# Kernel tuning notes

Measured on AMD Instinct MI355X. Metric: run time of the kernel, lower is better.

## Reference

```python
import jax, jax.numpy as jnp
import numpy as np

N, C, H, W = 16, 64, 128, 128
KH, KW = 3, 3
SH, SW = 1, 1


def _window_flat_indices(H, W):
    """Flat input indices of each element of each sliding window.
    Returns int32 array [num_windows, KH*KW]."""
    Ho = (H - KH) // SH + 1
    Wo = (W - KW) // SW + 1
    i = np.arange(Ho) * SH
    j = np.arange(Wo) * SW
    a = np.arange(KH)
    b = np.arange(KW)
    rows = i[:, None, None, None] + a[None, None, :, None]   # [Ho,1,KH,1]
    cols = j[None, :, None, None] + b[None, None, None, :]   # [1,Wo,1,KW]
    flat = (rows * W + cols).reshape(Ho * Wo, KH * KW)       # [Wn, K]
    return jnp.asarray(flat, dtype=jnp.int32)


def setup_inputs() -> dict:
    key = jax.random.key(0)
    x = jax.random.normal(key, (N, C, H, W), dtype=jnp.float32)
    return {"x": x}


def reference(x):
    n, c, h, w = x.shape
    flat = _window_flat_indices(h, w)            # [Wn, K]
    Wn, K = flat.shape
    nc = n * c
    xf = x.reshape(nc, h * w)                    # [NC, HW]
    patches = xf[:, flat]                        # [NC, Wn, K]
    amax = jnp.argmax(patches, axis=-1)          # [NC, Wn] local winner
    amin = jnp.argmin(patches, axis=-1)          # [NC, Wn]
    warp = jnp.arange(Wn)[None, :]
    win_max = flat[warp, amax]                   # [NC, Wn] flat input idx of max winner
    win_min = flat[warp, amin]                   # [NC, Wn]
    idx = jnp.concatenate([win_max, win_min], axis=1)                      # [NC, 2Wn]
    vals = jnp.concatenate([jnp.ones((Wn,), x.dtype), -jnp.ones((Wn,), x.dtype)])
    counts = jnp.zeros((nc, h * w), x.dtype)
    counts = counts.at[jnp.arange(nc)[:, None], idx].add(vals[None, :])
    return counts.reshape(n, c, h, w)
```

## Files before the change

kernel.cpp:

```cpp
#include <hip/hip_runtime.h>


#define HH 128
#define WW 128
#define HO 126
#define WO 126
#define PLANE (HH * WW)
#define NPLANES (16 * 64)
#define BLOCK 1024
#define CTILES 32
#define RTILES 63
#define NTILES (CTILES * RTILES)

__device__ __forceinline__ void scan9(float w0, float w1, float w2,
                                      float w3, float w4, float w5,
                                      float w6, float w7, float w8,
                                      int base, int* __restrict__ cnt) {
    float vmax = w0, vmin = w0;
    int omax = 0, omin = 0;
#define STEP(v, off)                                      \
    do {                                                  \
        if ((v) > vmax) { vmax = (v); omax = (off); }     \
        if ((v) < vmin) { vmin = (v); omin = (off); }     \
    } while (0)
    STEP(w1, 1);
    STEP(w2, 2);
    STEP(w3, WW);
    STEP(w4, WW + 1);
    STEP(w5, WW + 2);
    STEP(w6, 2 * WW);
    STEP(w7, 2 * WW + 1);
    STEP(w8, 2 * WW + 2);
#undef STEP
    atomicAdd(&cnt[base + omax], 1);
    atomicAdd(&cnt[base + omin], -1);
}

__global__ __launch_bounds__(BLOCK, 8)
void energy_pool2d_kernel(const float* __restrict__ x, float* __restrict__ out) {
    __shared__ int cnt[PLANE];

    const int tid = threadIdx.x;
    const int plane = blockIdx.x;
    const float* __restrict__ xp = x + (size_t)plane * PLANE;

    int4* c4 = (int4*)cnt;
#pragma unroll
    for (int i = 0; i < PLANE / 4 / BLOCK; ++i)
        c4[tid + i * BLOCK] = make_int4(0, 0, 0, 0);
    __syncthreads();

    for (int t = tid; t < NTILES; t += BLOCK) {
        const int rt = t >> 5;
        const int ct = t & 31;
        const int wr0 = rt * 2;
        const int j0 = ct * 4;
        const float* __restrict__ p = xp + wr0 * WW + j0;

        const float4 a0 = *(const float4*)(p);
        const float4 a1 = *(const float4*)(p + WW);
        const float4 a2 = *(const float4*)(p + 2 * WW);
        const float4 a3 = *(const float4*)(p + 3 * WW);
        float4 b0, b1, b2, b3;
        if (ct < CTILES - 1) {
            b0 = *(const float4*)(p + 4);
            b1 = *(const float4*)(p + WW + 4);
            b2 = *(const float4*)(p + 2 * WW + 4);
            b3 = *(const float4*)(p + 3 * WW + 4);
        } else {
            b0 = b1 = b2 = b3 = make_float4(0.f, 0.f, 0.f, 0.f);
        }
        const float r0[8] = {a0.x, a0.y, a0.z, a0.w, b0.x, b0.y, b0.z, b0.w};
        const float r1[8] = {a1.x, a1.y, a1.z, a1.w, b1.x, b1.y, b1.z, b1.w};
        const float r2[8] = {a2.x, a2.y, a2.z, a2.w, b2.x, b2.y, b2.z, b2.w};
        const float r3[8] = {a3.x, a3.y, a3.z, a3.w, b3.x, b3.y, b3.z, b3.w};

        const int nw = (ct < CTILES - 1) ? 4 : 2;
        const int base0 = wr0 * WW + j0;
#pragma unroll
        for (int c = 0; c < 4; ++c) {
            if (c < nw) {
                scan9(r0[c], r0[c + 1], r0[c + 2],
                      r1[c], r1[c + 1], r1[c + 2],
                      r2[c], r2[c + 1], r2[c + 2], base0 + c, cnt);
                scan9(r1[c], r1[c + 1], r1[c + 2],
                      r2[c], r2[c + 1], r2[c + 2],
                      r3[c], r3[c + 1], r3[c + 2], base0 + WW + c, cnt);
            }
        }
    }
    __syncthreads();

    float4* __restrict__ o4 = (float4*)(out + (size_t)plane * PLANE);
#pragma unroll
    for (int i = 0; i < PLANE / 4 / BLOCK; ++i) {
        const int4 ci = c4[tid + i * BLOCK];
        o4[tid + i * BLOCK] =
            make_float4((float)ci.x, (float)ci.y, (float)ci.z, (float)ci.w);
    }
}

extern "C" void kernel_launch(void* const* d_in, const int* in_sizes, int n_in,
                              void* d_out, int out_size, void* d_ws, size_t ws_size,
                              hipStream_t stream) {
    const float* x = (const float*)d_in[0];
    float* out = (float*)d_out;
    energy_pool2d_kernel<<<NPLANES, BLOCK, 0, stream>>>(x, out);
}
```

Baseline: 32.22 us.

## Split each plane across two blocks with halo rows and half-size LDS histogram

After: 32.31 us. Within noise of the previous version (+0.3%).

```diff
diff --git a/kernel.cpp b/kernel.cpp
--- a/kernel.cpp
+++ b/kernel.cpp
@@ -6,16 +6,15 @@
 #define HO 126
 #define WO 126
 #define PLANE (HH * WW)
+#define HROWS 64
+#define HPLANE (HROWS * WW)
 #define NPLANES (16 * 64)
-#define BLOCK 1024
-#define CTILES 32
-#define RTILES 63
-#define NTILES (CTILES * RTILES)
+#define BLOCK 512
 
 __device__ __forceinline__ void scan9(float w0, float w1, float w2,
                                       float w3, float w4, float w5,
                                       float w6, float w7, float w8,
-                                      int base, int* __restrict__ cnt) {
+                                      int base, int bias, int* __restrict__ cnt) {
     float vmax = w0, vmin = w0;
     int omax = 0, omin = 0;
 #define STEP(v, off)                                      \
@@ -32,28 +31,36 @@
     STEP(w7, 2 * WW + 1);
     STEP(w8, 2 * WW + 2);
 #undef STEP
-    atomicAdd(&cnt[base + omax], 1);
-    atomicAdd(&cnt[base + omin], -1);
+    const int iM = base + omax - bias;
+    if ((unsigned)iM < HPLANE) atomicAdd(&cnt[iM], 1);
+    const int im = base + omin - bias;
+    if ((unsigned)im < HPLANE) atomicAdd(&cnt[im], -1);
 }
 
 __global__ __launch_bounds__(BLOCK, 8)
 void energy_pool2d_kernel(const float* __restrict__ x, float* __restrict__ out) {
-    __shared__ int cnt[PLANE];
+    __shared__ int cnt[HPLANE];
 
     const int tid = threadIdx.x;
-    const int plane = blockIdx.x;
+    const int plane = blockIdx.x >> 1;
+    const int half = blockIdx.x & 1;
     const float* __restrict__ xp = x + (size_t)plane * PLANE;
 
     int4* c4 = (int4*)cnt;
 #pragma unroll
-    for (int i = 0; i < PLANE / 4 / BLOCK; ++i)
+    for (int i = 0; i < HPLANE / 4 / BLOCK; ++i)
         c4[tid + i * BLOCK] = make_int4(0, 0, 0, 0);
     __syncthreads();
 
-    for (int t = tid; t < NTILES; t += BLOCK) {
+    const int row0 = half ? 62 : 0;
+    const int bias = half * HPLANE;
+
+#pragma unroll
+    for (int it = 0; it < 2; ++it) {
+        const int t = tid + it * BLOCK;
         const int rt = t >> 5;
         const int ct = t & 31;
-        const int wr0 = rt * 2;
+        const int wr0 = row0 + rt * 2;
         const int j0 = ct * 4;
         const float* __restrict__ p = xp + wr0 * WW + j0;
 
@@ -62,7 +69,7 @@
         const float4 a2 = *(const float4*)(p + 2 * WW);
         const float4 a3 = *(const float4*)(p + 3 * WW);
         float4 b0, b1, b2, b3;
-        if (ct < CTILES - 1) {
+        if (ct < 31) {
             b0 = *(const float4*)(p + 4);
             b1 = *(const float4*)(p + WW + 4);
             b2 = *(const float4*)(p + 2 * WW + 4);
@@ -75,25 +82,25 @@
         const float r2[8] = {a2.x, a2.y, a2.z, a2.w, b2.x, b2.y, b2.z, b2.w};
         const float r3[8] = {a3.x, a3.y, a3.z, a3.w, b3.x, b3.y, b3.z, b3.w};
 
-        const int nw = (ct < CTILES - 1) ? 4 : 2;
+        const int nw = (ct < 31) ? 4 : 2;
         const int base0 = wr0 * WW + j0;
 #pragma unroll
         for (int c = 0; c < 4; ++c) {
             if (c < nw) {
                 scan9(r0[c], r0[c + 1], r0[c + 2],
                       r1[c], r1[c + 1], r1[c + 2],
-                      r2[c], r2[c + 1], r2[c + 2], base0 + c, cnt);
+                      r2[c], r2[c + 1], r2[c + 2], base0 + c, bias, cnt);
                 scan9(r1[c], r1[c + 1], r1[c + 2],
                       r2[c], r2[c + 1], r2[c + 2],
-                      r3[c], r3[c + 1], r3[c + 2], base0 + WW + c, cnt);
+                      r3[c], r3[c + 1], r3[c + 2], base0 + WW + c, bias, cnt);
             }
         }
     }
     __syncthreads();
 
-    float4* __restrict__ o4 = (float4*)(out + (size_t)plane * PLANE);
+    float4* __restrict__ o4 = (float4*)(out + (size_t)plane * PLANE + bias);
 #pragma unroll
-    for (int i = 0; i < PLANE / 4 / BLOCK; ++i) {
+    for (int i = 0; i < HPLANE / 4 / BLOCK; ++i) {
         const int4 ci = c4[tid + i * BLOCK];
         o4[tid + i * BLOCK] =
             make_float4((float)ci.x, (float)ci.y, (float)ci.z, (float)ci.w);
@@ -105,5 +112,5 @@
                               hipStream_t stream) {
     const float* x = (const float*)d_in[0];
     float* out = (float*)d_out;
-    energy_pool2d_kernel<<<NPLANES, BLOCK, 0, stream>>>(x, out);
+    energy_pool2d_kernel<<<NPLANES * 2, BLOCK, 0, stream>>>(x, out);
 }
```
